# Kernel optimization log

Hardware: AMD Instinct MI355X
Metric: run time of the kernel (lower is better)

## Reference

```python
import jax, jax.numpy as jnp
import numpy as np

LOG0 = -1e30


def _joint_logp(enc, pred, W_enc, W_pred, b_joint, W_out, b_out):
    # enc [B,T,De], pred [B,U+1,Dp] -> log-probs over full joint lattice [B,T,U+1,V]
    ep = jnp.einsum('btd,dj->btj', enc, W_enc)          # [B,T,J]
    pp = jnp.einsum('bud,dj->buj', pred, W_pred)        # [B,U+1,J]
    h = jnp.tanh(ep[:, :, None, :] + pp[:, None, :, :] + b_joint)  # [B,T,U+1,J]
    logits = jnp.einsum('btuj,jv->btuv', h, W_out) + b_out          # [B,T,U+1,V]
    return jax.nn.log_softmax(logits, axis=-1)


def _rnnt_loss(enc, pred, W_enc, W_pred, b_joint, W_out, b_out,
               labels, enc_lens, label_lens, blank_id):
    B, T, _ = enc.shape
    Up1 = pred.shape[1]
    U = Up1 - 1
    logp = _joint_logp(enc, pred, W_enc, W_pred, b_joint, W_out, b_out)
    blank_lp = logp[..., blank_id]                       # [B,T,U+1]
    # label_lp[b,t,u] = logp[b,t,u,labels[b,u]]
    label_lp = jnp.take_along_axis(
        logp[:, :, :U, :], labels[:, None, :, None], axis=3)[..., 0]  # [B,T,U]

    # alpha recurrence over t; the inner u-recurrence
    #   a[u] = logaddexp(alpha[u]+blank_lp[u], a[u-1]+label_lp[u-1])
    # is a log-space linear recurrence solved in parallel via cumlogsumexp:
    #   with L[u] = sum_{j<u} label_lp[j],  a = L + cumlogsumexp(c - L),  c = alpha + blank_lp
    def step(alpha, t):
        blp = blank_lp[:, t]                              # [B,U+1]
        llp = label_lp[:, t]                              # [B,U]
        c = alpha + blp
        L = jnp.concatenate(
            [jnp.zeros((B, 1), dtype=alpha.dtype), jnp.cumsum(llp, axis=1)], axis=1)
        a_new = L + jax.lax.cumlogsumexp(c - L, axis=1)
        alpha = jnp.where((t < enc_lens)[:, None], a_new, alpha)
        return alpha, None

    alpha0 = jnp.full((B, Up1), LOG0, dtype=enc.dtype).at[:, 0].set(0.0)
    alpha, _ = jax.lax.scan(step, alpha0, jnp.arange(T))

    bidx = jnp.arange(B)
    terminal_blank = blank_lp[bidx, enc_lens - 1, label_lens]   # [B]
    alpha_U = alpha[bidx, label_lens]                           # [B]
    return jnp.mean(-(alpha_U + terminal_blank))


def setup_inputs() -> dict:
    key = jax.random.key(0)
    ks = jax.random.split(key, 9)
    B, T, U = 8, 256, 64
    De, Dp, J, V = 640, 640, 512, 1024
    enc = jax.random.normal(ks[0], (B, T, De), dtype=jnp.float32)
    pred = jax.random.normal(ks[1], (B, U + 1, Dp), dtype=jnp.float32)
    labels = jax.random.randint(ks[2], (B, U), 1, V).astype(jnp.int32)
    enc_lens = jax.random.randint(ks[3], (B,), T // 2, T + 1).astype(jnp.int32)
    label_lens = jax.random.randint(ks[4], (B,), U // 2, U + 1).astype(jnp.int32)
    W_enc = jax.random.normal(ks[5], (De, J), dtype=jnp.float32) * (De ** -0.5)
    W_pred = jax.random.normal(ks[6], (Dp, J), dtype=jnp.float32) * (Dp ** -0.5)
    b_joint = jnp.zeros((J,), dtype=jnp.float32)
    W_out = jax.random.normal(ks[7], (J, V), dtype=jnp.float32) * (J ** -0.5)
    b_out = jnp.zeros((V,), dtype=jnp.float32)
    return {"enc": enc, "pred": pred, "W_enc": W_enc, "W_pred": W_pred,
            "b_joint": b_joint, "W_out": W_out, "b_out": b_out,
            "labels": labels, "enc_lens": enc_lens, "label_lens": label_lens,
            "blank_id": 0}


def reference(enc, pred, W_enc, W_pred, b_joint, W_out, b_out,
              labels, enc_lens, label_lens, blank_id):
    return _rnnt_loss(enc, pred, W_enc, W_pred, b_joint, W_out, b_out,
                      labels, enc_lens, label_lens, blank_id)
```

## Files before the change

kernel.cpp:

```cpp
#include <hip/hip_runtime.h>
#include <math.h>

#define B_   8
#define T_   256
#define U_   64
#define UP1  65
#define DE   640
#define J_   512
#define V_   1024
#define NCELL (B_ * T_ * UP1)
#define LOG0 -1e30f
#define NSEG 8
#define SEGLEN 32
#define MLD  66

typedef __attribute__((ext_vector_type(4))) float f32x4;
typedef __attribute__((ext_vector_type(8))) short short8;

__device__ __forceinline__ unsigned short f2bf(float x) {
    union { float f; unsigned int u; } c; c.f = x;
    unsigned int r = (c.u + 0x7fffu + ((c.u >> 16) & 1u)) >> 16;
    return (unsigned short)r;
}

template<int CTRL, int RM>
__device__ __forceinline__ float dppz(float x) {
    return __builtin_bit_cast(float,
        __builtin_amdgcn_update_dpp(0, __builtin_bit_cast(int, x), CTRL, RM, 0xf, false));
}
template<int CTRL, int RM>
__device__ __forceinline__ float dpps(float x) {
    int xi = __builtin_bit_cast(int, x);
    return __builtin_bit_cast(float,
        __builtin_amdgcn_update_dpp(xi, xi, CTRL, RM, 0xf, false));
}
__device__ __forceinline__ float wave_prefix_sum(float v) {
    v += dppz<0x111, 0xf>(v);
    v += dppz<0x112, 0xf>(v);
    v += dppz<0x114, 0xf>(v);
    v += dppz<0x118, 0xf>(v);
    v += dppz<0x142, 0xa>(v);
    v += dppz<0x143, 0xc>(v);
    return v;
}
__device__ __forceinline__ float wave_max_all(float v) {
    v = fmaxf(v, dpps<0x111, 0xf>(v));
    v = fmaxf(v, dpps<0x112, 0xf>(v));
    v = fmaxf(v, dpps<0x114, 0xf>(v));
    v = fmaxf(v, dpps<0x118, 0xf>(v));
    v = fmaxf(v, dpps<0x142, 0xa>(v));
    v = fmaxf(v, dpps<0x143, 0xc>(v));
    return __builtin_bit_cast(float,
        __builtin_amdgcn_readlane(__builtin_bit_cast(int, v), 63));
}
__device__ __forceinline__ float rdlane(float v, int l) {
    return __builtin_bit_cast(float,
        __builtin_amdgcn_readlane(__builtin_bit_cast(int, v), l));
}

__device__ __forceinline__ unsigned hb8(unsigned m, unsigned cb) {
    return m * 512u + (cb ^ ((m & 15u) << 3));
}

__global__ __launch_bounds__(256) void prep_kernel(const float* __restrict__ We,
                                                   const float* __restrict__ Wp,
                                                   const float* __restrict__ enc,
                                                   const float* __restrict__ pred,
                                                   unsigned short* __restrict__ wf2e,
                                                   unsigned short* __restrict__ wf2p,
                                                   unsigned short* __restrict__ encB,
                                                   unsigned short* __restrict__ predB) {
    int bx = blockIdx.x, tid = threadIdx.x;
    if (bx < 320) {
        const float* W = (bx < 160) ? We : Wp;
        unsigned short* dst = (bx < 160) ? wf2e : wf2p;
        int gid = ((bx < 160) ? bx : bx - 160) * 256 + tid;
        int lane = gid & 63, ktl = gid >> 6;
        int kt = ktl % 20, tl = ktl / 20;
        int lg = lane >> 4, ln = lane & 15;
        int col = tl * 16 + ln;
        short8 v;
#pragma unroll
        for (int j = 0; j < 8; ++j)
            v[j] = (short)f2bf(W[(size_t)(kt * 32 + lg * 8 + j) * J_ + col]);
        *(short8*)(dst + (size_t)gid * 8) = v;
    } else if (bx < 960) {
        int gid = (bx - 320) * 256 + tid;
        const float* s = enc + (size_t)gid * 8;
        float4 a = *(const float4*)s, b = *(const float4*)(s + 4);
        short8 v;
        v[0] = (short)f2bf(a.x); v[1] = (short)f2bf(a.y);
        v[2] = (short)f2bf(a.z); v[3] = (short)f2bf(a.w);
        v[4] = (short)f2bf(b.x); v[5] = (short)f2bf(b.y);
        v[6] = (short)f2bf(b.z); v[7] = (short)f2bf(b.w);
        *(short8*)(encB + (size_t)gid * 8) = v;
    } else {
        int gid = (bx - 960) * 256 + tid;
        if (gid < 41600) {
            const float* s = pred + (size_t)gid * 8;
            float4 a = *(const float4*)s, b = *(const float4*)(s + 4);
            short8 v;
            v[0] = (short)f2bf(a.x); v[1] = (short)f2bf(a.y);
            v[2] = (short)f2bf(a.z); v[3] = (short)f2bf(a.w);
            v[4] = (short)f2bf(b.x); v[5] = (short)f2bf(b.y);
            v[6] = (short)f2bf(b.z); v[7] = (short)f2bf(b.w);
            *(short8*)(predB + (size_t)gid * 8) = v;
        }
    }
}

__global__ __launch_bounds__(64) void gemm_mfma(const unsigned short* __restrict__ encB,
                                                const unsigned short* __restrict__ predB,
                                                const unsigned short* __restrict__ wf2e,
                                                const unsigned short* __restrict__ wf2p,
                                                const float* __restrict__ bj,
                                                float* __restrict__ ep,
                                                float* __restrict__ pp) {
    int rt = blockIdx.x, ct = blockIdx.y;
    int lane = threadIdx.x;
    const unsigned short* A;
    const short8* wp;
    float* C;
    const float* bias;
    int M, row0;
    if (rt < 32) { A = encB;  wp = (const short8*)wf2e; C = ep; bias = bj;      M = 2048; row0 = rt * 64; }
    else         { A = predB; wp = (const short8*)wf2p; C = pp; bias = nullptr; M = 520;  row0 = (rt - 32) * 64; }
    int lg = lane >> 4, ln = lane & 15;

    int r_[4];
#pragma unroll
    for (int mi = 0; mi < 4; ++mi) {
        int rr = row0 + mi * 16 + ln;
        r_[mi] = (rr < M) ? rr : (M - 1);
    }

#define WIDX(NI, KT) (((size_t)((ct * 4 + (NI)) * 20 + (KT))) * 64 + lane)
    short8 bf[3][4], af[2][4];
#pragma unroll
    for (int ni = 0; ni < 4; ++ni) bf[0][ni] = wp[WIDX(ni, 0)];
#pragma unroll
    for (int ni = 0; ni < 4; ++ni) bf[1][ni] = wp[WIDX(ni, 1)];
#pragma unroll
    for (int mi = 0; mi < 4; ++mi)
        af[0][mi] = *(const short8*)(A + (size_t)r_[mi] * DE + lg * 8);

    f32x4 acc[4][4] = {};
#pragma unroll
    for (int kt = 0; kt < 20; ++kt) {
        const int cur3 = kt % 3;
        const int pf3  = (kt + 2) % 3;
        const int cur  = kt & 1, nxt = cur ^ 1;
#pragma unroll
        for (int ni = 0; ni < 4; ++ni) {
            if (kt < 18) bf[pf3][ni] = wp[WIDX(ni, kt + 2)];
            __builtin_amdgcn_s_setprio(1);
#pragma unroll
            for (int mi = 0; mi < 4; ++mi)
                acc[mi][ni] = __builtin_amdgcn_mfma_f32_16x16x32_bf16(
                    af[cur][mi], bf[cur3][ni], acc[mi][ni], 0, 0, 0);
            __builtin_amdgcn_s_setprio(0);
            if (ni == 1 && kt < 19) {
#pragma unroll
                for (int mi = 0; mi < 4; ++mi)
                    af[nxt][mi] = *(const short8*)(A + (size_t)r_[mi] * DE +
                                                   (kt + 1) * 32 + lg * 8);
            }
        }
    }
#undef WIDX

#pragma unroll
    for (int mi = 0; mi < 4; ++mi) {
#pragma unroll
        for (int r = 0; r < 4; ++r) {
            int row = row0 + mi * 16 + lg * 4 + r;
            if (row >= M) continue;
#pragma unroll
            for (int ni = 0; ni < 4; ++ni) {
                int col = ct * 64 + ni * 16 + ln;
                float v = acc[mi][ni][r];
                if (bias) v += bias[col];
                C[(size_t)row * J_ + col] = v;
            }
        }
    }
}

__global__ __launch_bounds__(256) void wt_kernel(const float* __restrict__ W,
                                                 unsigned char* __restrict__ Wf) {
    __shared__ float tile[32][33];
    int tid = threadIdx.x;
    int tx = tid & 31, ty = tid >> 5;
    int v0 = blockIdx.x * 32, k0 = blockIdx.y * 32;
#pragma unroll
    for (int i = 0; i < 4; ++i)
        tile[ty + i * 8][tx] = W[(size_t)(k0 + ty + i * 8) * V_ + v0 + tx];
    __syncthreads();
    if (tid < 128) {
        int vl = tid >> 2, lg = tid & 3;
        int v  = v0 + vl;
        float x[8];
#pragma unroll
        for (int j = 0; j < 8; ++j) x[j] = tile[lg * 8 + j][vl];
        int lo = 0, hi = 0;
        lo = __builtin_amdgcn_cvt_pk_fp8_f32(x[0], x[1], lo, false);
        lo = __builtin_amdgcn_cvt_pk_fp8_f32(x[2], x[3], lo, true);
        hi = __builtin_amdgcn_cvt_pk_fp8_f32(x[4], x[5], hi, false);
        hi = __builtin_amdgcn_cvt_pk_fp8_f32(x[6], x[7], hi, true);
        int tl = v >> 4, ln = v & 15, kt = k0 >> 5;
        *(int2*)(Wf + tl * 8192 + kt * 512 + (lg * 16 + ln) * 8) = make_int2(lo, hi);
    }
}

__global__ __launch_bounds__(512) void hgen_kernel(const float* __restrict__ ep,
                                                   const float* __restrict__ pp,
                                                   unsigned char* __restrict__ hG) {
    int tid  = threadIdx.x;
    int tile = blockIdx.x;
    unsigned char* outb = hG + (size_t)tile * 32768;
#pragma unroll
    for (int i = 0; i < 4; ++i) {
        int g   = tid + i * 512;
        int row = g >> 5;
        int lin9 = (g & 31) * 16;
        unsigned swz = ((unsigned)(row & 15)) << 3;
        int k0   = lin9 ^ (int)(swz & ~8u);
        int swap = row & 1;
        int cell = tile * 64 + row;
        unsigned epRow = (unsigned)cell / 65u;
        int u = cell - (int)epRow * 65;
        int b = (int)(epRow >> 8);
        const float* epr = ep + (size_t)epRow * J_ + k0;
        const float* ppr = pp + (size_t)(b * UP1 + u) * J_ + k0;
        float t[16];
#pragma unroll
        for (int q = 0; q < 4; ++q) {
            float4 e = *(const float4*)(epr + q * 4);
            float4 p = *(const float4*)(ppr + q * 4);
            float xs[4] = {e.x + p.x, e.y + p.y, e.z + p.z, e.w + p.w};
#pragma unroll
            for (int j = 0; j < 4; ++j) {
                float e2 = __expf(2.f * xs[j]);
                t[q * 4 + j] = 1.f - 2.f / (e2 + 1.f);
            }
        }
        int a0 = 0, a1 = 0, b0 = 0, b1 = 0;
        a0 = __builtin_amdgcn_cvt_pk_fp8_f32(t[0], t[1], a0, false);
        a0 = __builtin_amdgcn_cvt_pk_fp8_f32(t[2], t[3], a0, true);
        a1 = __builtin_amdgcn_cvt_pk_fp8_f32(t[4], t[5], a1, false);
        a1 = __builtin_amdgcn_cvt_pk_fp8_f32(t[6], t[7], a1, true);
        b0 = __builtin_amdgcn_cvt_pk_fp8_f32(t[8], t[9], b0, false);
        b0 = __builtin_amdgcn_cvt_pk_fp8_f32(t[10], t[11], b0, true);
        b1 = __builtin_amdgcn_cvt_pk_fp8_f32(t[12], t[13], b1, false);
        b1 = __builtin_amdgcn_cvt_pk_fp8_f32(t[14], t[15], b1, true);
        int4 w = swap ? make_int4(b0, b1, a0, a1) : make_int4(a0, a1, b0, b1);
        *(int4*)(outb + g * 16) = w;
    }
}

__global__ __launch_bounds__(256, 3) void joint_mfma(const unsigned char* __restrict__ hG,
                                                     const unsigned char* __restrict__ Wf,
                                                     const float* __restrict__ bout,
                                                     const int* __restrict__ labels,
                                                     const int* __restrict__ pblank,
                                                     float* __restrict__ Spart,
                                                     float* __restrict__ blp,
                                                     float* __restrict__ llp) {
    __shared__ __align__(16) unsigned char hB[64 * 512];
    __shared__ float ps[4][64];

    int tid  = threadIdx.x;
    int bx   = blockIdx.x;
    int tile = (bx >> 5) * 8 + (bx & 7);
    int bh   = (bx >> 3) & 3;
    int c0   = tile * 64;
    int wc = tid >> 6, lane = tid & 63;
    int lg = lane >> 4, ln = lane & 15;

    const long* wfbL = (const long*)Wf + (((bh << 4) + (wc << 2)) << 10) + lane;

    long bf[3][4];
    long af[2][4];

    {
        int4 v[8];
        const int4* g = (const int4*)(hG + (size_t)tile * 32768) + tid;
#pragma unroll
        for (int i = 0; i < 8; ++i) v[i] = g[i * 256];
#pragma unroll
        for (int ni = 0; ni < 4; ++ni) bf[0][ni] = wfbL[ni * 1024];
#pragma unroll
        for (int ni = 0; ni < 4; ++ni) bf[1][ni] = wfbL[ni * 1024 + 64];
#pragma unroll
        for (int i = 0; i < 8; ++i) ((int4*)hB)[tid + i * 256] = v[i];
    }
    __syncthreads();

    f32x4 acc[4][4] = {};
#pragma unroll
    for (int mi = 0; mi < 4; ++mi)
        af[0][mi] = *(const long*)(hB + hb8((unsigned)(mi * 16 + ln), (unsigned)(lg * 8)));

#pragma unroll
    for (int kt = 0; kt < 16; ++kt) {
        const int cur3 = kt % 3;
        const int pf3  = (kt + 2) % 3;
        const int cur  = kt & 1, nxt = cur ^ 1;
#pragma unroll
        for (int ni = 0; ni < 4; ++ni) {
            if (kt < 14) bf[pf3][ni] = wfbL[ni * 1024 + (kt + 2) * 64];
            __builtin_amdgcn_s_setprio(1);
#pragma unroll
            for (int mi = 0; mi < 4; ++mi)
                acc[mi][ni] = __builtin_amdgcn_mfma_f32_16x16x32_fp8_fp8(
                    af[cur][mi], bf[cur3][ni], acc[mi][ni], 0, 0, 0);
            __builtin_amdgcn_s_setprio(0);
            if (ni == 1 && kt < 15) {
#pragma unroll
                for (int mi = 0; mi < 4; ++mi) {
                    unsigned m  = (unsigned)(mi * 16 + ln);
                    unsigned cb = (unsigned)((kt + 1) * 32 + lg * 8);
                    af[nxt][mi] = *(const long*)(hB + hb8(m, cb));
                }
            }
        }
    }

    float bo[4];
#pragma unroll
    for (int ni = 0; ni < 4; ++ni) bo[ni] = bout[(bh << 8) + (wc << 6) + (ni << 4) + ln];
#pragma unroll
    for (int mi = 0; mi < 4; ++mi)
#pragma unroll
        for (int ni = 0; ni < 4; ++ni)
#pragma unroll
            for (int r = 0; r < 4; ++r) acc[mi][ni][r] += bo[ni];

#pragma unroll
    for (int mi = 0; mi < 4; ++mi) {
#pragma unroll
        for (int r = 0; r < 4; ++r) {
            float s = 0.f;
#pragma unroll
            for (int ni = 0; ni < 4; ++ni) s += __expf(acc[mi][ni][r]);
            s += __shfl_xor(s, 1);
            s += __shfl_xor(s, 2);
            s += __shfl_xor(s, 4);
            s += __shfl_xor(s, 8);
            if (ln == 0) ps[wc][mi * 16 + lg * 4 + r] = s;
        }
    }
    __syncthreads();
    if (tid < 64) {
        float S = ps[0][tid] + ps[1][tid] + ps[2][tid] + ps[3][tid];
        Spart[(size_t)bh * NCELL + c0 + tid] = S;
    }

    int blank = *pblank;
#pragma unroll
    for (int mi = 0; mi < 4; ++mi) {
#pragma unroll
        for (int r = 0; r < 4; ++r) {
            int row  = mi * 16 + lg * 4 + r;
            int cell = c0 + row;
            unsigned epRow = (unsigned)cell / 65u;
            int u = cell - (int)epRow * 65;
            int b = (int)(epRow >> 8);
            int lab = (u < U_) ? labels[(b << 6) + u] : -1;
#pragma unroll
            for (int ni = 0; ni < 4; ++ni) {
                int col = (bh << 8) + (wc << 6) + (ni << 4) + ln;
                float lgt = acc[mi][ni][r];
                if (col == blank) blp[cell] = lgt;
                if (col == lab)   llp[(size_t)(((int)epRow << 6) + u)] = lgt;
            }
        }
    }
}

__global__ __launch_bounds__(256) void pass2_kernel(const float* __restrict__ Spart,
                                                    float* __restrict__ blp,
                                                    float* __restrict__ llp) {
    int idx = blockIdx.x * 256 + threadIdx.x;
    if (idx >= NCELL) return;
    float lse = __logf(Spart[idx] + Spart[NCELL + idx] +
                       Spart[2 * NCELL + idx] + Spart[3 * NCELL + idx]);
    blp[idx] -= lse;
    unsigned epRow = (unsigned)idx / 65u;
    int u = idx - (int)epRow * 65;
    if (u < U_) llp[(size_t)((epRow << 6) + u)] -= lse;
}

__global__ __launch_bounds__(64) void segscan_kernel(const float* __restrict__ blp,
                                                     const float* __restrict__ llp,
                                                     const int* __restrict__ enc_lens,
                                                     float* __restrict__ Mbuf) {
    const float K2 = 1.4426950408889634f;
    int idx  = blockIdx.x;
    int v    = idx % 65;
    int seg  = (idx / 65) % NSEG;
    int b    = idx / (65 * NSEG);
    int lane = threadIdx.x;
    int el   = enc_lens[b];
    int t0   = seg * SEGLEN;
    if (t0 >= el) return;
    const float* bb = blp + (size_t)b * T_ * UP1;
    const float* lb = llp + (size_t)b * T_ * U_;

    float bvK[SEGLEN], lvK[SEGLEN], b64K[SEGLEN];
#pragma unroll
    for (int j = 0; j < SEGLEN; ++j) {
        int t  = t0 + j;
        int tc = (t < el) ? t : (el - 1);
        bvK[j]  = bb[tc * UP1 + lane] * K2;
        b64K[j] = bb[tc * UP1 + 64] * K2;
        lvK[j]  = lb[tc * U_ + lane] * K2;
    }

    float alpha   = (lane == v) ? 0.f : LOG0;
    float alpha64 = (v == 64) ? 0.f : LOG0;

#pragma unroll
    for (int j = 0; j < SEGLEN; ++j) {
        if (t0 + j < el) {
            float P = wave_prefix_sum(lvK[j]);
            float L = dpps<0x111, 0xf>(P);
            float P15 = rdlane(P, 15), P31 = rdlane(P, 31), P47 = rdlane(P, 47);
            if (lane == 0)  L = 0.f;
            if (lane == 16) L = P15;
            if (lane == 32) L = P31;
            if (lane == 48) L = P47;
            float P63 = rdlane(P, 63);
            float x   = alpha + bvK[j] - L;
            float x64 = alpha64 + b64K[j] - P63;
            float M = fmaxf(wave_max_all(x), x64);
            float S = wave_prefix_sum(__builtin_amdgcn_exp2f(x - M));
            float S63 = rdlane(S, 63);
            alpha   = L + M + __builtin_amdgcn_logf(S);
            alpha64 = P63 + M +
                      __builtin_amdgcn_logf(S63 + __builtin_amdgcn_exp2f(x64 - M));
        }
    }

    float* col = Mbuf + ((size_t)((b * NSEG + seg) * 65 + v)) * MLD;
    col[lane] = fmaxf(alpha, LOG0);
    if (lane == 0) col[64] = fmaxf(alpha64, LOG0);
}

__global__ __launch_bounds__(64) void apply_kernel(const float* __restrict__ Mbuf,
                                                   const float* __restrict__ blp,
                                                   const int* __restrict__ enc_lens,
                                                   const int* __restrict__ label_lens,
                                                   float* __restrict__ lossBuf) {
    __shared__ float Ml[65 * MLD];
    __shared__ float xv[66];
    const float K2  = 1.4426950408889634f;
    const float LN2 = 0.6931471805599453f;
    int b    = blockIdx.x;
    int lane = threadIdx.x;
    int el = enc_lens[b];
    int ll = label_lens[b];

    xv[lane] = (lane == 0) ? 0.f : LOG0;
    if (lane == 0) xv[64] = LOG0;
    __syncthreads();

    for (int seg = 0; seg < NSEG; ++seg) {
        if (seg * SEGLEN >= el) break;
        const float* src = Mbuf + (size_t)((b * NSEG + seg) * 65) * MLD;
        for (int i = lane; i < 65 * MLD; i += 64) Ml[i] = src[i];
        __syncthreads();
        float m = LOG0;
#pragma unroll 5
        for (int vv = 0; vv < 65; ++vv) m = fmaxf(m, Ml[vv * MLD + lane] + xv[vv]);
        m = fmaxf(m, LOG0);
        float s = 0.f;
#pragma unroll 5
        for (int vv = 0; vv < 65; ++vv)
            s += __builtin_amdgcn_exp2f(Ml[vv * MLD + lane] + xv[vv] - m);
        float y = fmaxf(m + __builtin_amdgcn_logf(s), LOG0);
        float t64  = xv[lane] + Ml[lane * MLD + 64];
        float t64b = xv[64] + Ml[64 * MLD + 64];
        float m64 = fmaxf(fmaxf(wave_max_all(t64), t64b), LOG0);
        float s64 = rdlane(wave_prefix_sum(__builtin_amdgcn_exp2f(t64 - m64)), 63);
        s64 += __builtin_amdgcn_exp2f(t64b - m64);
        float y64 = fmaxf(m64 + __builtin_amdgcn_logf(s64), LOG0);
        __syncthreads();
        xv[lane] = y;
        if (lane == 0) xv[64] = y64;
        __syncthreads();
    }

    if (lane == 0) {
        float aU = (ll < 64) ? xv[ll] : xv[64];
        float term = blp[(size_t)b * T_ * UP1 + (el - 1) * UP1 + ll] * K2;
        lossBuf[b] = -(aU + term) * LN2;
    }
}

__global__ __launch_bounds__(64) void finalize_kernel(const float* __restrict__ lossBuf,
                                                      float* __restrict__ out) {
    if (threadIdx.x == 0) {
        float s = 0.f;
        for (int i = 0; i < B_; ++i) s += lossBuf[i];
        out[0] = s / (float)B_;
    }
}

extern "C" void kernel_launch(void* const* d_in, const int* in_sizes, int n_in,
                              void* d_out, int out_size, void* d_ws, size_t ws_size,
                              hipStream_t stream) {
    (void)in_sizes; (void)n_in; (void)out_size; (void)ws_size;
    const float* enc        = (const float*)d_in[0];
    const float* pred       = (const float*)d_in[1];
    const float* W_enc      = (const float*)d_in[2];
    const float* W_pred     = (const float*)d_in[3];
    const float* b_joint    = (const float*)d_in[4];
    const float* W_out      = (const float*)d_in[5];
    const float* b_out      = (const float*)d_in[6];
    const int*   labels     = (const int*)d_in[7];
    const int*   enc_lens   = (const int*)d_in[8];
    const int*   label_lens = (const int*)d_in[9];
    const int*   blank_id   = (const int*)d_in[10];

    float* ep  = (float*)d_ws;
    float* pp  = ep  + (size_t)B_ * T_ * J_;
    float* blp = pp  + (size_t)B_ * UP1 * J_;
    float* llp = blp + (size_t)B_ * T_ * UP1;
    unsigned char* Wf = (unsigned char*)(llp + (size_t)B_ * T_ * U_);
    float* Spart = (float*)(Wf + (size_t)V_ * J_);
    unsigned char* hG = (unsigned char*)(Spart + (size_t)4 * NCELL);
    float* lossBuf = (float*)(hG + (size_t)NCELL * 512);
    float* Mbuf    = lossBuf + 64;

    unsigned short* encB  = (unsigned short*)hG;
    unsigned short* predB = encB + (size_t)2048 * DE;
    unsigned short* wf2e  = predB + (size_t)520 * DE;
    unsigned short* wf2p  = wf2e + (size_t)DE * J_;

    wt_kernel<<<dim3(V_ / 32, J_ / 32), dim3(256), 0, stream>>>(W_out, Wf);
    prep_kernel<<<dim3(1123), dim3(256), 0, stream>>>(W_enc, W_pred, enc, pred,
                                                      wf2e, wf2p, encB, predB);
    gemm_mfma<<<dim3(41, 8), dim3(64), 0, stream>>>(encB, predB, wf2e, wf2p, b_joint,
                                                    ep, pp);
    hgen_kernel<<<dim3(NCELL / 64), dim3(512), 0, stream>>>(ep, pp, hG);
    joint_mfma<<<dim3(NCELL / 64 * 4), dim3(256), 0, stream>>>(
        hG, Wf, b_out, labels, blank_id, Spart, blp, llp);
    pass2_kernel<<<dim3((NCELL + 255) / 256), dim3(256), 0, stream>>>(Spart, blp, llp);
    segscan_kernel<<<dim3(B_ * NSEG * 65), dim3(64), 0, stream>>>(blp, llp, enc_lens,
                                                                  Mbuf);
    apply_kernel<<<dim3(B_), dim3(64), 0, stream>>>(Mbuf, blp, enc_lens, label_lens,
                                                    lossBuf);
    finalize_kernel<<<dim3(1), dim3(64), 0, stream>>>(lossBuf, (float*)d_out);
}
```

Baseline: 268.0 us.

## Emit h in MFMA fragment layout and load A operands directly from global

hgen now writes the fp8 hidden activations already arranged in per-lane MFMA A-fragment order, so joint_mfma can read A fragments straight from global memory with a three-deep register prefetch. This removes the 32KB LDS staging buffer, its swizzle, and the block barrier. The W_out fp8 transpose is folded into prep_kernel as extra blocks, which saves one kernel launch. In exchange, the four column-waves of a tile each reload the same A data from global or L2 instead of sharing it through LDS.

```diff
diff --git a/kernel.cpp b/kernel.cpp
--- a/kernel.cpp
+++ b/kernel.cpp
@@ -58,18 +58,16 @@
         __builtin_amdgcn_readlane(__builtin_bit_cast(int, v), l));
 }
 
-__device__ __forceinline__ unsigned hb8(unsigned m, unsigned cb) {
-    return m * 512u + (cb ^ ((m & 15u) << 3));
-}
-
 __global__ __launch_bounds__(256) void prep_kernel(const float* __restrict__ We,
                                                    const float* __restrict__ Wp,
                                                    const float* __restrict__ enc,
                                                    const float* __restrict__ pred,
+                                                   const float* __restrict__ Wout,
                                                    unsigned short* __restrict__ wf2e,
                                                    unsigned short* __restrict__ wf2p,
                                                    unsigned short* __restrict__ encB,
-                                                   unsigned short* __restrict__ predB) {
+                                                   unsigned short* __restrict__ predB,
+                                                   unsigned char* __restrict__ Wf) {
     int bx = blockIdx.x, tid = threadIdx.x;
     if (bx < 320) {
         const float* W = (bx < 160) ? We : Wp;
@@ -94,7 +92,7 @@
         v[4] = (short)f2bf(b.x); v[5] = (short)f2bf(b.y);
         v[6] = (short)f2bf(b.z); v[7] = (short)f2bf(b.w);
         *(short8*)(encB + (size_t)gid * 8) = v;
-    } else {
+    } else if (bx < 1123) {
         int gid = (bx - 960) * 256 + tid;
         if (gid < 41600) {
             const float* s = pred + (size_t)gid * 8;
@@ -105,6 +103,29 @@
             v[4] = (short)f2bf(b.x); v[5] = (short)f2bf(b.y);
             v[6] = (short)f2bf(b.z); v[7] = (short)f2bf(b.w);
             *(short8*)(predB + (size_t)gid * 8) = v;
+        }
+    } else {
+        __shared__ float tile[32][33];
+        int bx2 = bx - 1123;
+        int tx = tid & 31, ty = tid >> 5;
+        int v0 = (bx2 & 31) * 32, k0 = (bx2 >> 5) * 32;
+#pragma unroll
+        for (int i = 0; i < 4; ++i)
+            tile[ty + i * 8][tx] = Wout[(size_t)(k0 + ty + i * 8) * V_ + v0 + tx];
+        __syncthreads();
+        if (tid < 128) {
+            int vl = tid >> 2, lg = tid & 3;
+            int v  = v0 + vl;
+            float x[8];
+#pragma unroll
+            for (int j = 0; j < 8; ++j) x[j] = tile[lg * 8 + j][vl];
+            int lo = 0, hi = 0;
+            lo = __builtin_amdgcn_cvt_pk_fp8_f32(x[0], x[1], lo, false);
+            lo = __builtin_amdgcn_cvt_pk_fp8_f32(x[2], x[3], lo, true);
+            hi = __builtin_amdgcn_cvt_pk_fp8_f32(x[4], x[5], hi, false);
+            hi = __builtin_amdgcn_cvt_pk_fp8_f32(x[6], x[7], hi, true);
+            int tl = v >> 4, ln = v & 15, kt = k0 >> 5;
+            *(int2*)(Wf + tl * 8192 + kt * 512 + (lg * 16 + ln) * 8) = make_int2(lo, hi);
         }
     }
 }
@@ -186,75 +207,43 @@
     }
 }
 
-__global__ __launch_bounds__(256) void wt_kernel(const float* __restrict__ W,
-                                                 unsigned char* __restrict__ Wf) {
-    __shared__ float tile[32][33];
-    int tid = threadIdx.x;
-    int tx = tid & 31, ty = tid >> 5;
-    int v0 = blockIdx.x * 32, k0 = blockIdx.y * 32;
-#pragma unroll
-    for (int i = 0; i < 4; ++i)
-        tile[ty + i * 8][tx] = W[(size_t)(k0 + ty + i * 8) * V_ + v0 + tx];
-    __syncthreads();
-    if (tid < 128) {
-        int vl = tid >> 2, lg = tid & 3;
-        int v  = v0 + vl;
-        float x[8];
-#pragma unroll
-        for (int j = 0; j < 8; ++j) x[j] = tile[lg * 8 + j][vl];
-        int lo = 0, hi = 0;
-        lo = __builtin_amdgcn_cvt_pk_fp8_f32(x[0], x[1], lo, false);
-        lo = __builtin_amdgcn_cvt_pk_fp8_f32(x[2], x[3], lo, true);
-        hi = __builtin_amdgcn_cvt_pk_fp8_f32(x[4], x[5], hi, false);
-        hi = __builtin_amdgcn_cvt_pk_fp8_f32(x[6], x[7], hi, true);
-        int tl = v >> 4, ln = v & 15, kt = k0 >> 5;
-        *(int2*)(Wf + tl * 8192 + kt * 512 + (lg * 16 + ln) * 8) = make_int2(lo, hi);
-    }
-}
-
 __global__ __launch_bounds__(512) void hgen_kernel(const float* __restrict__ ep,
                                                    const float* __restrict__ pp,
                                                    unsigned char* __restrict__ hG) {
     int tid  = threadIdx.x;
     int tile = blockIdx.x;
-    unsigned char* outb = hG + (size_t)tile * 32768;
-#pragma unroll
-    for (int i = 0; i < 4; ++i) {
-        int g   = tid + i * 512;
-        int row = g >> 5;
-        int lin9 = (g & 31) * 16;
-        unsigned swz = ((unsigned)(row & 15)) << 3;
-        int k0   = lin9 ^ (int)(swz & ~8u);
-        int swap = row & 1;
+    long* outb = (long*)(hG + (size_t)tile * 32768);
+#pragma unroll
+    for (int i = 0; i < 8; ++i) {
+        int q    = tid + i * 512;
+        int lane = q & 63;
+        int ktmi = q >> 6;
+        int kt = ktmi & 15, mi = ktmi >> 4;
+        int ln = lane & 15, lg = lane >> 4;
+        int row = mi * 16 + ln;
+        int k   = kt * 32 + lg * 8;
         int cell = tile * 64 + row;
         unsigned epRow = (unsigned)cell / 65u;
         int u = cell - (int)epRow * 65;
         int b = (int)(epRow >> 8);
-        const float* epr = ep + (size_t)epRow * J_ + k0;
-        const float* ppr = pp + (size_t)(b * UP1 + u) * J_ + k0;
-        float t[16];
-#pragma unroll
-        for (int q = 0; q < 4; ++q) {
-            float4 e = *(const float4*)(epr + q * 4);
-            float4 p = *(const float4*)(ppr + q * 4);
-            float xs[4] = {e.x + p.x, e.y + p.y, e.z + p.z, e.w + p.w};
-#pragma unroll
-            for (int j = 0; j < 4; ++j) {
-                float e2 = __expf(2.f * xs[j]);
-                t[q * 4 + j] = 1.f - 2.f / (e2 + 1.f);
-            }
-        }
-        int a0 = 0, a1 = 0, b0 = 0, b1 = 0;
-        a0 = __builtin_amdgcn_cvt_pk_fp8_f32(t[0], t[1], a0, false);
-        a0 = __builtin_amdgcn_cvt_pk_fp8_f32(t[2], t[3], a0, true);
-        a1 = __builtin_amdgcn_cvt_pk_fp8_f32(t[4], t[5], a1, false);
-        a1 = __builtin_amdgcn_cvt_pk_fp8_f32(t[6], t[7], a1, true);
-        b0 = __builtin_amdgcn_cvt_pk_fp8_f32(t[8], t[9], b0, false);
-        b0 = __builtin_amdgcn_cvt_pk_fp8_f32(t[10], t[11], b0, true);
-        b1 = __builtin_amdgcn_cvt_pk_fp8_f32(t[12], t[13], b1, false);
-        b1 = __builtin_amdgcn_cvt_pk_fp8_f32(t[14], t[15], b1, true);
-        int4 w = swap ? make_int4(b0, b1, a0, a1) : make_int4(a0, a1, b0, b1);
-        *(int4*)(outb + g * 16) = w;
+        const float* epr = ep + (size_t)epRow * J_ + k;
+        const float* ppr = pp + (size_t)(b * UP1 + u) * J_ + k;
+        float4 e0 = *(const float4*)epr, e1 = *(const float4*)(epr + 4);
+        float4 p0 = *(const float4*)ppr, p1 = *(const float4*)(ppr + 4);
+        float x[8] = {e0.x + p0.x, e0.y + p0.y, e0.z + p0.z, e0.w + p0.w,
+                      e1.x + p1.x, e1.y + p1.y, e1.z + p1.z, e1.w + p1.w};
+        float t[8];
+#pragma unroll
+        for (int j = 0; j < 8; ++j) {
+            float e2 = __expf(2.f * x[j]);
+            t[j] = 1.f - 2.f / (e2 + 1.f);
+        }
+        int lo = 0, hi = 0;
+        lo = __builtin_amdgcn_cvt_pk_fp8_f32(t[0], t[1], lo, false);
+        lo = __builtin_amdgcn_cvt_pk_fp8_f32(t[2], t[3], lo, true);
+        hi = __builtin_amdgcn_cvt_pk_fp8_f32(t[4], t[5], hi, false);
+        hi = __builtin_amdgcn_cvt_pk_fp8_f32(t[6], t[7], hi, true);
+        outb[q] = ((long)(unsigned)hi << 32) | (unsigned)lo;
     }
 }
 
@@ -266,7 +255,6 @@
                                                      float* __restrict__ Spart,
                                                      float* __restrict__ blp,
                                                      float* __restrict__ llp) {
-    __shared__ __align__(16) unsigned char hB[64 * 512];
     __shared__ float ps[4][64];
 
     int tid  = threadIdx.x;
@@ -277,52 +265,39 @@
     int wc = tid >> 6, lane = tid & 63;
     int lg = lane >> 4, ln = lane & 15;
 
+    const long* hf   = (const long*)(hG + (size_t)tile * 32768) + lane;
     const long* wfbL = (const long*)Wf + (((bh << 4) + (wc << 2)) << 10) + lane;
 
     long bf[3][4];
-    long af[2][4];
-
-    {
-        int4 v[8];
-        const int4* g = (const int4*)(hG + (size_t)tile * 32768) + tid;
-#pragma unroll
-        for (int i = 0; i < 8; ++i) v[i] = g[i * 256];
-#pragma unroll
-        for (int ni = 0; ni < 4; ++ni) bf[0][ni] = wfbL[ni * 1024];
-#pragma unroll
-        for (int ni = 0; ni < 4; ++ni) bf[1][ni] = wfbL[ni * 1024 + 64];
-#pragma unroll
-        for (int i = 0; i < 8; ++i) ((int4*)hB)[tid + i * 256] = v[i];
-    }
-    __syncthreads();
+    long af[3][4];
+#pragma unroll
+    for (int ni = 0; ni < 4; ++ni) bf[0][ni] = wfbL[ni * 1024];
+#pragma unroll
+    for (int ni = 0; ni < 4; ++ni) bf[1][ni] = wfbL[ni * 1024 + 64];
+#pragma unroll
+    for (int mi = 0; mi < 4; ++mi) af[0][mi] = hf[(mi << 10)];
+#pragma unroll
+    for (int mi = 0; mi < 4; ++mi) af[1][mi] = hf[(mi << 10) + 64];
 
     f32x4 acc[4][4] = {};
-#pragma unroll
-    for (int mi = 0; mi < 4; ++mi)
-        af[0][mi] = *(const long*)(hB + hb8((unsigned)(mi * 16 + ln), (unsigned)(lg * 8)));
-
 #pragma unroll
     for (int kt = 0; kt < 16; ++kt) {
         const int cur3 = kt % 3;
         const int pf3  = (kt + 2) % 3;
-        const int cur  = kt & 1, nxt = cur ^ 1;
 #pragma unroll
         for (int ni = 0; ni < 4; ++ni) {
+            if (ni == 0 && kt < 14) {
+#pragma unroll
+                for (int mi = 0; mi < 4; ++mi)
+                    af[pf3][mi] = hf[(mi << 10) + ((kt + 2) << 6)];
+            }
             if (kt < 14) bf[pf3][ni] = wfbL[ni * 1024 + (kt + 2) * 64];
             __builtin_amdgcn_s_setprio(1);
 #pragma unroll
             for (int mi = 0; mi < 4; ++mi)
                 acc[mi][ni] = __builtin_amdgcn_mfma_f32_16x16x32_fp8_fp8(
-                    af[cur][mi], bf[cur3][ni], acc[mi][ni], 0, 0, 0);
+                    af[cur3][mi], bf[cur3][ni], acc[mi][ni], 0, 0, 0);
             __builtin_amdgcn_s_setprio(0);
-            if (ni == 1 && kt < 15) {
-#pragma unroll
-                for (int mi = 0; mi < 4; ++mi) {
-                    unsigned m  = (unsigned)(mi * 16 + ln);
-                    unsigned cb = (unsigned)((kt + 1) * 32 + lg * 8);
-                    af[nxt][mi] = *(const long*)(hB + hb8(m, cb));
-                }
-            }
         }
     }
 
@@ -538,9 +513,8 @@
     unsigned short* wf2e  = predB + (size_t)520 * DE;
     unsigned short* wf2p  = wf2e + (size_t)DE * J_;
 
-    wt_kernel<<<dim3(V_ / 32, J_ / 32), dim3(256), 0, stream>>>(W_out, Wf);
-    prep_kernel<<<dim3(1123), dim3(256), 0, stream>>>(W_enc, W_pred, enc, pred,
-                                                      wf2e, wf2p, encB, predB);
+    prep_kernel<<<dim3(1635), dim3(256), 0, stream>>>(W_enc, W_pred, enc, pred, W_out,
+                                                      wf2e, wf2p, encB, predB, Wf);
     gemm_mfma<<<dim3(41, 8), dim3(64), 0, stream>>>(encB, predB, wf2e, wf2p, b_joint,
                                                     ep, pp);
     hgen_kernel<<<dim3(NCELL / 64), dim3(512), 0, stream>>>(ep, pp, hG);
```

New measurement: 321.4 us. +19.9%, slower.
